# Kernel optimization log

Measured on AMD Instinct MI355X. Metric: run time of the kernel, lower is better.

## Reference

```python
import jax, jax.numpy as jnp
import numpy as np

DIM = 1024
K = 9            # kernel_size
PAD = 4          # padding = (K-1)//2


def setup_inputs() -> dict:
    key = jax.random.key(0)
    k1, k2, k3, k4, k5 = jax.random.split(key, 5)
    b, l, d = 4, 4096, DIM
    s = 1.0 / np.sqrt(d)
    x = jax.random.normal(k1, (b, l, d), dtype=jnp.float32)
    # linear2: dim -> k^2 + k   (torch Linear: y = x @ W.T + b)
    w2 = jax.random.uniform(k2, (K * K + K, d), jnp.float32, -s, s)
    b2 = jax.random.uniform(k3, (K * K + K,), jnp.float32, -s, s)
    # outlinear: dim -> dim
    wo = jax.random.uniform(k4, (d, d), jnp.float32, -s, s)
    bo = jax.random.uniform(k5, (d,), jnp.float32, -s, s)
    return {"x": x, "w2": w2, "b2": b2, "wo": wo, "bo": bo}


def reference(x, w2, b2, wo, bo):
    b, l, d = x.shape
    # per-token generated weights / bias
    att = x @ w2.T + b2                                  # (b, l, k^2 + k)
    aw = jnp.sin(att[..., : K * K]).reshape(b, l, K, K)  # (b, l, k, k)
    ab = att[..., K * K :]                               # (b, l, k)
    # sliding windows along sequence: (b, l, d, k)
    xp = jnp.pad(x, ((0, 0), (PAD, PAD), (0, 0)))
    windows = jnp.stack([xp[:, i : i + l] for i in range(K)], axis=-1)
    # sum_j (windows @ aw)[..., j] == windows @ aw.sum(-1); bias sums over k, broadcast over d
    y = jnp.einsum("bldk,blk->bld", windows, aw.sum(axis=-1)) + ab.sum(axis=-1, keepdims=True)
    return y @ wo.T + bo
```

## Files before the change

### kernel.cpp

```cpp
#include <hip/hip_runtime.h>
#include <hip/hip_bf16.h>

#define DIM   1024
#define SEQL  4096
#define NTOK  16384
#define NATT  90
#define NATTP 96

typedef __attribute__((ext_vector_type(8))) short frag_ab;
typedef __attribute__((ext_vector_type(4))) float frag_cd;

typedef unsigned int u32;
typedef const __attribute__((address_space(1))) u32* gp_t;
typedef __attribute__((address_space(3))) u32* lp_t;

static __device__ __forceinline__ unsigned short f2bf(float f) {
    unsigned int u = __float_as_uint(f);
    return (unsigned short)((u + 0x7fffu + ((u >> 16) & 1u)) >> 16);
}
static __device__ __forceinline__ ushort4 f4tobf(float4 v) {
    ushort4 r; r.x = f2bf(v.x); r.y = f2bf(v.y); r.z = f2bf(v.z); r.w = f2bf(v.w);
    return r;
}
static __device__ __forceinline__ float4 bf4tof(ushort4 u) {
    float4 r;
    r.x = __uint_as_float((u32)u.x << 16);
    r.y = __uint_as_float((u32)u.y << 16);
    r.z = __uint_as_float((u32)u.z << 16);
    r.w = __uint_as_float((u32)u.w << 16);
    return r;
}

__global__ __launch_bounds__(256) void cvt_kernel(
    const float* __restrict__ w2, const float* __restrict__ wo,
    unsigned short* __restrict__ w2p, unsigned short* __restrict__ wob)
{
    const int bid = blockIdx.x;
    if (bid < 1024) {
        const int i = bid * 256 + threadIdx.x;
        float4 v = ((const float4*)wo)[i];
        *(ushort4*)(wob + (size_t)i * 4) = f4tobf(v);
    } else {
        const int idx = (bid - 1024) * 256 + threadIdx.x;
        const int c    = idx / 384;
        const int rem  = idx - c * 384;
        const int f    = rem >> 6;
        const int lane = rem & 63;
        const int row  = f * 16 + (lane & 15);
        const int col  = c * 32 + (lane >> 4) * 8;
        float4 v0 = make_float4(0.f, 0.f, 0.f, 0.f), v1 = v0;
        if (row < NATT) {
            v0 = *(const float4*)(w2 + (size_t)row * DIM + col);
            v1 = *(const float4*)(w2 + (size_t)row * DIM + col + 4);
        }
        unsigned short* dst = w2p + (size_t)idx * 8;
        *(ushort4*)(dst)     = f4tobf(v0);
        *(ushort4*)(dst + 4) = f4tobf(v1);
    }
}

#define ATOK 16
#define PSTR 98

__global__ __launch_bounds__(256) void att_y_kernel(
    const float* __restrict__ x, const unsigned short* __restrict__ w2p,
    const float* __restrict__ b2, unsigned short* __restrict__ ybf)
{
    __shared__ __align__(16) unsigned short xs[ATOK * 1024];
    __shared__ float part[2 * ATOK * PSTR];
    __shared__ float summ[ATOK * NATTP];
    __shared__ float b2s[NATTP];
    __shared__ float coe[ATOK][12];

    const int tid  = threadIdx.x;
    const int wave = tid >> 6, lane = tid & 63;
    const int fr = lane & 15, kq = lane >> 4;
    const int tok0 = blockIdx.x * ATOK;
    const int bb = tok0 >> 12;
    const int l0 = tok0 & 4095;

    if (tid < NATTP) b2s[tid] = (tid < NATT) ? b2[tid] : 0.f;

    #pragma unroll
    for (int t = 0; t < 4; ++t) {
        const int row = t * 4 + wave;
        const float4* xr = (const float4*)(x + (size_t)(tok0 + row) * DIM);
        #pragma unroll
        for (int tt = 0; tt < 4; ++tt) {
            const int c4 = tt * 64 + lane;
            float4 v = xr[c4];
            const int ch = c4 >> 1, half = c4 & 1;
            *(ushort4*)(&xs[row * 1024 + ((ch ^ (row & 7)) * 8 + half * 4)]) = f4tobf(v);
        }
    }

    const float4 z4 = make_float4(0.f, 0.f, 0.f, 0.f);
    float4 halo[8];
    #pragma unroll
    for (int hh = 0; hh < 8; ++hh) {
        const int off = (hh < 4) ? (hh - 4) : (hh + 12);
        const int src = l0 + off;
        halo[hh] = z4;
        if (src >= 0 && src < SEQL)
            halo[hh] = *((const float4*)(x + ((size_t)bb * SEQL + src) * DIM) + tid);
    }
    __syncthreads();

    frag_cd acc[6] = {};
    #pragma unroll
    for (int kk = 0; kk < 8; ++kk) {
        const int ch = wave * 32 + kk * 4 + kq;
        frag_ab a = *(const frag_ab*)(&xs[fr * 1024 + ((ch ^ (fr & 7)) * 8)]);
        const int c = wave * 8 + kk;
        #pragma unroll
        for (int f = 0; f < 6; ++f) {
            frag_ab b = *(const frag_ab*)(w2p + ((size_t)((c * 6 + f) * 64) + lane) * 8);
            acc[f] = __builtin_amdgcn_mfma_f32_16x16x32_bf16(a, b, acc[f], 0, 0, 0);
        }
    }

    const int col = lane & 15, rb = (lane >> 4) * 4;
    float* myp = &part[(wave & 1) * ATOK * PSTR];
    if (wave < 2) {
        #pragma unroll
        for (int f = 0; f < 6; ++f)
            #pragma unroll
            for (int r = 0; r < 4; ++r)
                myp[(rb + r) * PSTR + f * 16 + col] = acc[f][r];
    }
    __syncthreads();
    if (wave >= 2) {
        #pragma unroll
        for (int f = 0; f < 6; ++f)
            #pragma unroll
            for (int r = 0; r < 4; ++r)
                myp[(rb + r) * PSTR + f * 16 + col] += acc[f][r];
    }
    __syncthreads();

    for (int o = tid; o < ATOK * NATTP; o += 256) {
        const int t = o / NATTP, m = o - (o / NATTP) * NATTP;
        summ[o] = b2s[m] + part[t * PSTR + m] + part[ATOK * PSTR + t * PSTR + m];
    }
    __syncthreads();

    if (tid < 160) {
        const int t = tid / 10, j = tid - (tid / 10) * 10;
        float s = 0.f;
        if (j < 9) {
            #pragma unroll
            for (int jj = 0; jj < 9; ++jj) s += sinf(summ[t * NATTP + j * 9 + jj]);
        } else {
            #pragma unroll
            for (int m = NATT - 9; m < NATT; ++m) s += summ[t * NATTP + m];
        }
        coe[t][j] = s;
    }
    __syncthreads();

    const int ch2 = tid >> 1, hf2 = tid & 1;
    auto rowval = [&](int rel) -> float4 {
        if (rel < 0)  return halo[rel + 4];
        if (rel > 15) return halo[rel - 12];
        ushort4 u = *(const ushort4*)(&xs[rel * 1024 + ((ch2 ^ (rel & 7)) * 8 + hf2 * 4)]);
        return bf4tof(u);
    };

    float4 w[9];
    #pragma unroll
    for (int k = 0; k < 8; ++k) w[k] = rowval(k - 4);

    #pragma unroll
    for (int t = 0; t < ATOK; ++t) {
        w[8] = rowval(t + 4);
        float4 a4;
        a4.x = a4.y = a4.z = a4.w = coe[t][9];
        #pragma unroll
        for (int k = 0; k < 9; ++k) {
            const float ck = coe[t][k];
            a4.x += ck * w[k].x; a4.y += ck * w[k].y;
            a4.z += ck * w[k].z; a4.w += ck * w[k].w;
        }
        *(ushort4*)(ybf + (size_t)(tok0 + t) * DIM + tid * 4) = f4tobf(a4);
        #pragma unroll
        for (int k = 0; k < 8; ++k) w[k] = w[k + 1];
    }
}

#define GBM 256
#define GBN 256
#define GBK 64

#define STAGE(d, kt)                                                           \
    {                                                                          \
        const int kc_ = (kt) * GBK;                                            \
        _Pragma("unroll")                                                      \
        for (int j_ = 0; j_ < 4; ++j_) {                                       \
            __builtin_amdgcn_global_load_lds(                                  \
                (gp_t)(A + (size_t)(m0 + srow[j_]) * DIM + kc_ + scol[j_]),    \
                (lp_t)(&As[d][(wave * 4 + j_) * 512]), 16, 0, 0);              \
            __builtin_amdgcn_global_load_lds(                                  \
                (gp_t)(Bm + (size_t)(n0 + srow[j_]) * DIM + kc_ + scol[j_]),   \
                (lp_t)(&Bs[d][(wave * 4 + j_) * 512]), 16, 0, 0);              \
        }                                                                      \
    }

__global__ __launch_bounds__(512, 2) void gemm_kernel(
    const unsigned short* __restrict__ A,
    const unsigned short* __restrict__ Bm,
    const float* __restrict__ bo,
    float* __restrict__ out)
{
    __shared__ unsigned short As[2][GBM * GBK];
    __shared__ unsigned short Bs[2][GBN * GBK];

    const int tid  = threadIdx.x;
    const int wave = tid >> 6, lane = tid & 63;
    const int fr = lane & 15, kq = lane >> 4;
    const int wm = (wave >> 2) * 128;
    const int wn = (wave & 3) * 64;

    const int bid = blockIdx.x;
    const int lid = (bid & 7) * 32 + (bid >> 3);
    const int m0  = (lid >> 2) * GBM;
    const int n0  = (lid & 3) * GBN;

    int srow[4], scol[4];
    #pragma unroll
    for (int j = 0; j < 4; ++j) {
        int ci = (wave * 4 + j) * 64 + lane;
        int row = ci >> 3;
        srow[j] = row;
        scol[j] = ((ci & 7) ^ (row & 7)) * 8;
    }

    frag_cd acc[8][4] = {};

    STAGE(0, 0);
    STAGE(1, 1);

    for (int kt = 0; kt < 15; ++kt) {
        const int d = kt & 1;
        asm volatile("s_waitcnt vmcnt(8)" ::: "memory");
        __builtin_amdgcn_s_barrier();

        frag_ab b0[4], b1[4];
        #pragma unroll
        for (int ni = 0; ni < 4; ++ni) {
            int row = wn + ni * 16 + fr;
            b0[ni] = *(const frag_ab*)(&Bs[d][row * 64 + ((kq       ^ (row & 7)) * 8)]);
            b1[ni] = *(const frag_ab*)(&Bs[d][row * 64 + (((4 + kq) ^ (row & 7)) * 8)]);
        }
        frag_ab alo0[4], alo1[4];
        #pragma unroll
        for (int mi = 0; mi < 4; ++mi) {
            int row = wm + mi * 16 + fr;
            alo0[mi] = *(const frag_ab*)(&As[d][row * 64 + ((kq       ^ (row & 7)) * 8)]);
            alo1[mi] = *(const frag_ab*)(&As[d][row * 64 + (((4 + kq) ^ (row & 7)) * 8)]);
        }
        __builtin_amdgcn_s_setprio(1);
        #pragma unroll
        for (int mi = 0; mi < 4; ++mi)
            #pragma unroll
            for (int ni = 0; ni < 4; ++ni) {
                acc[mi][ni] = __builtin_amdgcn_mfma_f32_16x16x32_bf16(alo0[mi], b0[ni], acc[mi][ni], 0, 0, 0);
                acc[mi][ni] = __builtin_amdgcn_mfma_f32_16x16x32_bf16(alo1[mi], b1[ni], acc[mi][ni], 0, 0, 0);
            }
        __builtin_amdgcn_s_setprio(0);
        frag_ab ahi0[4], ahi1[4];
        #pragma unroll
        for (int mi = 0; mi < 4; ++mi) {
            int row = wm + (mi + 4) * 16 + fr;
            ahi0[mi] = *(const frag_ab*)(&As[d][row * 64 + ((kq       ^ (row & 7)) * 8)]);
            ahi1[mi] = *(const frag_ab*)(&As[d][row * 64 + (((4 + kq) ^ (row & 7)) * 8)]);
        }
        asm volatile("s_waitcnt lgkmcnt(0)" ::: "memory");
        __builtin_amdgcn_s_barrier();
        if (kt < 14) { STAGE(d, kt + 2); }
        __builtin_amdgcn_s_setprio(1);
        #pragma unroll
        for (int mi = 0; mi < 4; ++mi)
            #pragma unroll
            for (int ni = 0; ni < 4; ++ni) {
                acc[mi + 4][ni] = __builtin_amdgcn_mfma_f32_16x16x32_bf16(ahi0[mi], b0[ni], acc[mi + 4][ni], 0, 0, 0);
                acc[mi + 4][ni] = __builtin_amdgcn_mfma_f32_16x16x32_bf16(ahi1[mi], b1[ni], acc[mi + 4][ni], 0, 0, 0);
            }
        __builtin_amdgcn_s_setprio(0);
    }

    {
        asm volatile("s_waitcnt vmcnt(0)" ::: "memory");
        __builtin_amdgcn_s_barrier();
        frag_ab b0[4], b1[4];
        #pragma unroll
        for (int ni = 0; ni < 4; ++ni) {
            int row = wn + ni * 16 + fr;
            b0[ni] = *(const frag_ab*)(&Bs[1][row * 64 + ((kq       ^ (row & 7)) * 8)]);
            b1[ni] = *(const frag_ab*)(&Bs[1][row * 64 + (((4 + kq) ^ (row & 7)) * 8)]);
        }
        #pragma unroll
        for (int h = 0; h < 2; ++h) {
            frag_ab a0[4], a1[4];
            #pragma unroll
            for (int mi = 0; mi < 4; ++mi) {
                int row = wm + (mi + h * 4) * 16 + fr;
                a0[mi] = *(const frag_ab*)(&As[1][row * 64 + ((kq       ^ (row & 7)) * 8)]);
                a1[mi] = *(const frag_ab*)(&As[1][row * 64 + (((4 + kq) ^ (row & 7)) * 8)]);
            }
            __builtin_amdgcn_s_setprio(1);
            #pragma unroll
            for (int mi = 0; mi < 4; ++mi)
                #pragma unroll
                for (int ni = 0; ni < 4; ++ni) {
                    acc[mi + h * 4][ni] = __builtin_amdgcn_mfma_f32_16x16x32_bf16(a0[mi], b0[ni], acc[mi + h * 4][ni], 0, 0, 0);
                    acc[mi + h * 4][ni] = __builtin_amdgcn_mfma_f32_16x16x32_bf16(a1[mi], b1[ni], acc[mi + h * 4][ni], 0, 0, 0);
                }
            __builtin_amdgcn_s_setprio(0);
        }
    }

    const int colb = lane & 15, rb = (lane >> 4) * 4;
    #pragma unroll
    for (int ni = 0; ni < 4; ++ni) {
        const int col = n0 + wn + ni * 16 + colb;
        const float bias = bo[col];
        #pragma unroll
        for (int mi = 0; mi < 8; ++mi) {
            #pragma unroll
            for (int r = 0; r < 4; ++r) {
                const int row = m0 + wm + mi * 16 + rb + r;
                out[(size_t)row * DIM + col] = acc[mi][ni][r] + bias;
            }
        }
    }
}

extern "C" void kernel_launch(void* const* d_in, const int* in_sizes, int n_in,
                              void* d_out, int out_size, void* d_ws, size_t ws_size,
                              hipStream_t stream) {
    const float* x  = (const float*)d_in[0];
    const float* w2 = (const float*)d_in[1];
    const float* b2 = (const float*)d_in[2];
    const float* wo = (const float*)d_in[3];
    const float* bo = (const float*)d_in[4];
    float* out = (float*)d_out;

    char* ws = (char*)d_ws;
    unsigned short* wob = (unsigned short*)ws;
    unsigned short* ybf = (unsigned short*)(ws + 2097152);
    unsigned short* w2p = (unsigned short*)(ws + 2097152 + 33554432);

    cvt_kernel<<<1024 + 48, 256, 0, stream>>>(w2, wo, w2p, wob);
    att_y_kernel<<<NTOK / ATOK, 256, 0, stream>>>(x, w2p, b2, ybf);
    gemm_kernel<<<NTOK / GBM * (DIM / GBN), 512, 0, stream>>>(ybf, wob, bo, out);
}
```

Before: 77.80 us.

## Split GEMM K-tile into half-slices with finer-grained interleaved load/MFMA schedule

```diff
diff --git a/kernel.cpp b/kernel.cpp
--- a/kernel.cpp
+++ b/kernel.cpp
@@ -187,23 +187,47 @@
     }
 }
 
-#define GBM 256
-#define GBN 256
-#define GBK 64
-
-#define STAGE(d, kt)                                                           \
-    {                                                                          \
-        const int kc_ = (kt) * GBK;                                            \
+
+#define VMC6 asm volatile("s_waitcnt vmcnt(6)" ::: "memory")
+#define VMC4 asm volatile("s_waitcnt vmcnt(4)" ::: "memory")
+#define VMC0 asm volatile("s_waitcnt vmcnt(0)" ::: "memory")
+#define LGKM0 asm volatile("s_waitcnt lgkmcnt(0)" ::: "memory")
+#define BAR  __builtin_amdgcn_s_barrier()
+
+#define STG(Ms, gbase, goff, dd, s_, kt_) {                                    \
+    _Pragma("unroll")                                                          \
+    for (int j_ = 0; j_ < 2; ++j_) {                                           \
+        const int idx_ = j_ * 512 + tid;                                       \
+        const int r_ = idx_ >> 2;                                              \
+        const int c_ = (idx_ & 3) ^ (r_ & 3);                                  \
+        __builtin_amdgcn_global_load_lds(                                      \
+            (gp_t)(gbase + (size_t)(goff + r_) * DIM + (kt_) * 64 + (s_) * 32 + c_ * 8), \
+            (lp_t)(&Ms[dd][s_][idx_ * 8]), 16, 0, 0);                          \
+    } }
+
+#define RDB(dd, s_, dst) {                                                     \
+    _Pragma("unroll")                                                          \
+    for (int ni_ = 0; ni_ < 4; ++ni_) {                                        \
+        const int r_ = wn + ni_ * 16 + fr;                                     \
+        dst[ni_] = *(const frag_ab*)(&Bs[dd][s_][r_ * 32 + ((kq ^ (r_ & 3)) * 8)]); \
+    } }
+
+#define RDA(dd, s_, g_, dst) {                                                 \
+    _Pragma("unroll")                                                          \
+    for (int mi_ = 0; mi_ < 4; ++mi_) {                                        \
+        const int r_ = wm + (g_) * 64 + mi_ * 16 + fr;                         \
+        dst[mi_] = *(const frag_ab*)(&As[dd][s_][r_ * 32 + ((kq ^ (r_ & 3)) * 8)]); \
+    } }
+
+#define MFMA16(base_, av_, bv_)                                                \
+    __builtin_amdgcn_s_setprio(1);                                             \
+    _Pragma("unroll")                                                          \
+    for (int mi_ = 0; mi_ < 4; ++mi_)                                          \
         _Pragma("unroll")                                                      \
-        for (int j_ = 0; j_ < 4; ++j_) {                                       \
-            __builtin_amdgcn_global_load_lds(                                  \
-                (gp_t)(A + (size_t)(m0 + srow[j_]) * DIM + kc_ + scol[j_]),    \
-                (lp_t)(&As[d][(wave * 4 + j_) * 512]), 16, 0, 0);              \
-            __builtin_amdgcn_global_load_lds(                                  \
-                (gp_t)(Bm + (size_t)(n0 + srow[j_]) * DIM + kc_ + scol[j_]),   \
-                (lp_t)(&Bs[d][(wave * 4 + j_) * 512]), 16, 0, 0);              \
-        }                                                                      \
-    }
+        for (int ni_ = 0; ni_ < 4; ++ni_)                                      \
+            acc[(base_) + mi_][ni_] = __builtin_amdgcn_mfma_f32_16x16x32_bf16( \
+                av_[mi_], bv_[ni_], acc[(base_) + mi_][ni_], 0, 0, 0);         \
+    __builtin_amdgcn_s_setprio(0);
 
 __global__ __launch_bounds__(512, 2) void gemm_kernel(
     const unsigned short* __restrict__ A,
@@ -211,8 +235,8 @@
     const float* __restrict__ bo,
     float* __restrict__ out)
 {
-    __shared__ unsigned short As[2][GBM * GBK];
-    __shared__ unsigned short Bs[2][GBN * GBK];
+    __shared__ unsigned short As[2][2][256 * 32];
+    __shared__ unsigned short Bs[2][2][256 * 32];
 
     const int tid  = threadIdx.x;
     const int wave = tid >> 6, lane = tid & 63;
@@ -222,101 +246,72 @@
 
     const int bid = blockIdx.x;
     const int lid = (bid & 7) * 32 + (bid >> 3);
-    const int m0  = (lid >> 2) * GBM;
-    const int n0  = (lid & 3) * GBN;
-
-    int srow[4], scol[4];
-    #pragma unroll
-    for (int j = 0; j < 4; ++j) {
-        int ci = (wave * 4 + j) * 64 + lane;
-        int row = ci >> 3;
-        srow[j] = row;
-        scol[j] = ((ci & 7) ^ (row & 7)) * 8;
-    }
+    const int m0  = (lid >> 2) * 256;
+    const int n0  = (lid & 3) * 256;
 
     frag_cd acc[8][4] = {};
 
-    STAGE(0, 0);
-    STAGE(1, 1);
-
-    for (int kt = 0; kt < 15; ++kt) {
-        const int d = kt & 1;
-        asm volatile("s_waitcnt vmcnt(8)" ::: "memory");
-        __builtin_amdgcn_s_barrier();
-
-        frag_ab b0[4], b1[4];
-        #pragma unroll
-        for (int ni = 0; ni < 4; ++ni) {
-            int row = wn + ni * 16 + fr;
-            b0[ni] = *(const frag_ab*)(&Bs[d][row * 64 + ((kq       ^ (row & 7)) * 8)]);
-            b1[ni] = *(const frag_ab*)(&Bs[d][row * 64 + (((4 + kq) ^ (row & 7)) * 8)]);
-        }
-        frag_ab alo0[4], alo1[4];
-        #pragma unroll
-        for (int mi = 0; mi < 4; ++mi) {
-            int row = wm + mi * 16 + fr;
-            alo0[mi] = *(const frag_ab*)(&As[d][row * 64 + ((kq       ^ (row & 7)) * 8)]);
-            alo1[mi] = *(const frag_ab*)(&As[d][row * 64 + (((4 + kq) ^ (row & 7)) * 8)]);
-        }
-        __builtin_amdgcn_s_setprio(1);
-        #pragma unroll
-        for (int mi = 0; mi < 4; ++mi)
-            #pragma unroll
-            for (int ni = 0; ni < 4; ++ni) {
-                acc[mi][ni] = __builtin_amdgcn_mfma_f32_16x16x32_bf16(alo0[mi], b0[ni], acc[mi][ni], 0, 0, 0);
-                acc[mi][ni] = __builtin_amdgcn_mfma_f32_16x16x32_bf16(alo1[mi], b1[ni], acc[mi][ni], 0, 0, 0);
-            }
-        __builtin_amdgcn_s_setprio(0);
-        frag_ab ahi0[4], ahi1[4];
-        #pragma unroll
-        for (int mi = 0; mi < 4; ++mi) {
-            int row = wm + (mi + 4) * 16 + fr;
-            ahi0[mi] = *(const frag_ab*)(&As[d][row * 64 + ((kq       ^ (row & 7)) * 8)]);
-            ahi1[mi] = *(const frag_ab*)(&As[d][row * 64 + (((4 + kq) ^ (row & 7)) * 8)]);
-        }
-        asm volatile("s_waitcnt lgkmcnt(0)" ::: "memory");
-        __builtin_amdgcn_s_barrier();
-        if (kt < 14) { STAGE(d, kt + 2); }
-        __builtin_amdgcn_s_setprio(1);
-        #pragma unroll
-        for (int mi = 0; mi < 4; ++mi)
-            #pragma unroll
-            for (int ni = 0; ni < 4; ++ni) {
-                acc[mi + 4][ni] = __builtin_amdgcn_mfma_f32_16x16x32_bf16(ahi0[mi], b0[ni], acc[mi + 4][ni], 0, 0, 0);
-                acc[mi + 4][ni] = __builtin_amdgcn_mfma_f32_16x16x32_bf16(ahi1[mi], b1[ni], acc[mi + 4][ni], 0, 0, 0);
-            }
-        __builtin_amdgcn_s_setprio(0);
+    STG(Bs, Bm, n0, 0, 0, 0);
+    STG(As, A,  m0, 0, 0, 0);
+    STG(Bs, Bm, n0, 0, 1, 0);
+    STG(As, A,  m0, 0, 1, 0);
+    VMC4;
+    BAR;
+
+    #pragma unroll 1
+    for (int t = 0; t < 15; ++t) {
+        const int d = t & 1, e = d ^ 1;
+        frag_ab b0[4], b1[4], av[4], aw[4];
+        RDB(d, 0, b0);
+        RDA(d, 0, 0, av);
+        STG(Bs, Bm, n0, e, 0, t + 1);
+        BAR;
+        LGKM0;
+        MFMA16(0, av, b0);
+        RDA(d, 0, 1, aw);
+        STG(As, A, m0, e, 0, t + 1);
+        BAR;
+        LGKM0;
+        MFMA16(4, aw, b0);
+        STG(Bs, Bm, n0, e, 1, t + 1);
+        VMC6;
+        BAR;
+        RDB(d, 1, b1);
+        RDA(d, 1, 0, av);
+        STG(As, A, m0, e, 1, t + 1);
+        BAR;
+        LGKM0;
+        MFMA16(0, av, b1);
+        RDA(d, 1, 1, aw);
+        BAR;
+        LGKM0;
+        MFMA16(4, aw, b1);
+        VMC4;
+        BAR;
     }
 
     {
-        asm volatile("s_waitcnt vmcnt(0)" ::: "memory");
-        __builtin_amdgcn_s_barrier();
-        frag_ab b0[4], b1[4];
-        #pragma unroll
-        for (int ni = 0; ni < 4; ++ni) {
-            int row = wn + ni * 16 + fr;
-            b0[ni] = *(const frag_ab*)(&Bs[1][row * 64 + ((kq       ^ (row & 7)) * 8)]);
-            b1[ni] = *(const frag_ab*)(&Bs[1][row * 64 + (((4 + kq) ^ (row & 7)) * 8)]);
-        }
-        #pragma unroll
-        for (int h = 0; h < 2; ++h) {
-            frag_ab a0[4], a1[4];
-            #pragma unroll
-            for (int mi = 0; mi < 4; ++mi) {
-                int row = wm + (mi + h * 4) * 16 + fr;
-                a0[mi] = *(const frag_ab*)(&As[1][row * 64 + ((kq       ^ (row & 7)) * 8)]);
-                a1[mi] = *(const frag_ab*)(&As[1][row * 64 + (((4 + kq) ^ (row & 7)) * 8)]);
-            }
-            __builtin_amdgcn_s_setprio(1);
-            #pragma unroll
-            for (int mi = 0; mi < 4; ++mi)
-                #pragma unroll
-                for (int ni = 0; ni < 4; ++ni) {
-                    acc[mi + h * 4][ni] = __builtin_amdgcn_mfma_f32_16x16x32_bf16(a0[mi], b0[ni], acc[mi + h * 4][ni], 0, 0, 0);
-                    acc[mi + h * 4][ni] = __builtin_amdgcn_mfma_f32_16x16x32_bf16(a1[mi], b1[ni], acc[mi + h * 4][ni], 0, 0, 0);
-                }
-            __builtin_amdgcn_s_setprio(0);
-        }
+        frag_ab b0[4], b1[4], av[4], aw[4];
+        RDB(1, 0, b0);
+        RDA(1, 0, 0, av);
+        BAR;
+        LGKM0;
+        MFMA16(0, av, b0);
+        RDA(1, 0, 1, aw);
+        BAR;
+        LGKM0;
+        MFMA16(4, aw, b0);
+        VMC0;
+        BAR;
+        RDB(1, 1, b1);
+        RDA(1, 1, 0, av);
+        BAR;
+        LGKM0;
+        MFMA16(0, av, b1);
+        RDA(1, 1, 1, aw);
+        BAR;
+        LGKM0;
+        MFMA16(4, aw, b1);
     }
 
     const int colb = lane & 15, rb = (lane >> 4) * 4;
@@ -352,5 +347,5 @@
 
     cvt_kernel<<<1024 + 48, 256, 0, stream>>>(w2, wo, w2p, wob);
     att_y_kernel<<<NTOK / ATOK, 256, 0, stream>>>(x, w2p, b2, ybf);
-    gemm_kernel<<<NTOK / GBM * (DIM / GBN), 512, 0, stream>>>(ybf, wob, bo, out);
-}
+    gemm_kernel<<<NTOK / 256 * (DIM / 256), 512, 0, stream>>>(ybf, wob, bo, out);
+}
```

Result: slower. 81.03 us (+4.2%).
